# Kernel tuning notes

Measured on AMD Instinct MI355X. Metric: run time of the kernel, lower is better.

The kernel has to match this reference:

```python
import jax, jax.numpy as jnp
import numpy as np

N_QUBITS = 4
N_LAYERS = 2
ENT = [(i, (i + 1) % N_QUBITS) for i in range(N_QUBITS)]  # fixed entangling ring


def _ry(t):
    c, s = jnp.cos(t / 2), jnp.sin(t / 2)
    return jnp.stack([jnp.stack([c, -s]), jnp.stack([s, c])]).astype(jnp.complex64)


def _rx(t):
    c, s = jnp.cos(t / 2), jnp.sin(t / 2)
    return jnp.stack([jnp.stack([c + 0j, -1j * s]), jnp.stack([-1j * s, c + 0j])]).astype(jnp.complex64)


def _rz(t):
    e = jnp.exp(-0.5j * t.astype(jnp.complex64))
    z = jnp.zeros_like(e)
    return jnp.stack([jnp.stack([e, z]), jnp.stack([z, jnp.conj(e)])])


def _apply_1q(state, U, w):
    # state: (2,)*N_QUBITS; apply 2x2 U on wire w
    s = jnp.moveaxis(state, w, 0)
    s = jnp.tensordot(U, s, ((1,), (0,)))
    return jnp.moveaxis(s, 0, w)


def _cnot(state, c, t):
    s = jnp.moveaxis(state, (c, t), (0, 1))
    s = jnp.concatenate([s[:1], jnp.flip(s[1:], axis=1)], axis=0)
    return jnp.moveaxis(s, (0, 1), (c, t))


def _ansatz(state, vec, params):
    for i in range(N_QUBITS):
        state = _apply_1q(state, _ry(vec[i]), i)
    for l in range(N_LAYERS):
        for i in range(N_QUBITS):
            state = _apply_1q(state, _rx(params[l, i, 0]), i)
            state = _apply_1q(state, _ry(params[l, i, 1]), i)
            state = _apply_1q(state, _rz(params[l, i, 2]), i)
        for a_, b_ in ENT:
            state = _cnot(state, a_, b_)
    return state


def _adjoint_ansatz(state, vec, params):
    # inverse gates in reverse order
    for l in reversed(range(N_LAYERS)):
        for a_, b_ in reversed(ENT):
            state = _cnot(state, a_, b_)  # CNOT is self-inverse
        for i in reversed(range(N_QUBITS)):
            state = _apply_1q(state, _rz(-params[l, i, 2]), i)
            state = _apply_1q(state, _ry(-params[l, i, 1]), i)
            state = _apply_1q(state, _rx(-params[l, i, 0]), i)
    for i in reversed(range(N_QUBITS)):
        state = _apply_1q(state, _ry(-vec[i]), i)
    return state


def setup_inputs() -> dict:
    key = jax.random.key(0)
    k1, k2, k3 = jax.random.split(key, 3)
    a = jax.random.normal(k1, (1024, N_QUBITS), dtype=jnp.float32)
    b = jax.random.normal(k2, (1024, N_QUBITS), dtype=jnp.float32)
    params = jax.random.normal(k3, (N_LAYERS, N_QUBITS, 3), dtype=jnp.float32)
    return {"a": a, "b": b, "params": params}


def reference(a, b, params):
    def pair(x, y):
        psi = jnp.zeros((2,) * N_QUBITS, jnp.complex64).at[(0,) * N_QUBITS].set(1.0)
        psi = _ansatz(psi, x, params)
        psi = _adjoint_ansatz(psi, y, params)
        probs = jnp.abs(psi) ** 2
        # expval of PauliZ on wire 0: +1 for |0>, -1 for |1> on axis 0
        z = jnp.sum(probs[0]) - jnp.sum(probs[1])
        return jnp.abs(z)

    # Gram matrix [len(a), len(b)]
    return jax.vmap(lambda x: jax.vmap(lambda y: pair(x, y))(b))(a)
```

## Files before the change

### kernel.cpp

```cpp
#include <hip/hip_runtime.h>


#define NA 1024
#define NB 1024
#define KD 256
#define RT2 1.41421356237f

typedef __attribute__((ext_vector_type(8))) short bf16x8;
typedef __attribute__((ext_vector_type(4))) float f32x4;

__device__ __forceinline__ unsigned short f2bf(float x) {
    union { float f; unsigned u; } v; v.f = x;
    unsigned r = v.u + 0x7fffu + ((v.u >> 16) & 1u);
    return (unsigned short)(r >> 16);
}

__device__ __forceinline__ uint4 pack8(const float* f) {
    uint4 u;
    u.x = (unsigned)f2bf(f[0]) | ((unsigned)f2bf(f[1]) << 16);
    u.y = (unsigned)f2bf(f[2]) | ((unsigned)f2bf(f[3]) << 16);
    u.z = (unsigned)f2bf(f[4]) | ((unsigned)f2bf(f[5]) << 16);
    u.w = (unsigned)f2bf(f[6]) | ((unsigned)f2bf(f[7]) << 16);
    return u;
}

__device__ __forceinline__ void ry_gate(float* sr, float* si, int w, float t) {
    float s, c; __sincosf(0.5f * t, &s, &c);
    int st = 8 >> w;
    #pragma unroll
    for (int b = 0; b < 16; ++b) {
        if (b & st) continue;
        int j = b | st;
        float r0 = sr[b], i0 = si[b], r1 = sr[j], i1 = si[j];
        sr[b] = c * r0 - s * r1;  si[b] = c * i0 - s * i1;
        sr[j] = s * r0 + c * r1;  si[j] = s * i0 + c * i1;
    }
}

__device__ __forceinline__ void rx_gate(float* sr, float* si, int w, float t) {
    float s, c; __sincosf(0.5f * t, &s, &c);
    int st = 8 >> w;
    #pragma unroll
    for (int b = 0; b < 16; ++b) {
        if (b & st) continue;
        int j = b | st;
        float r0 = sr[b], i0 = si[b], r1 = sr[j], i1 = si[j];
        sr[b] = c * r0 + s * i1;  si[b] = c * i0 - s * r1;
        sr[j] = c * r1 + s * i0;  si[j] = c * i1 - s * r0;
    }
}

__device__ __forceinline__ void rz_gate(float* sr, float* si, int w, float t) {
    float s, c; __sincosf(0.5f * t, &s, &c);
    int st = 8 >> w;
    #pragma unroll
    for (int b = 0; b < 16; ++b) {
        if (b & st) continue;
        int j = b | st;
        float r0 = sr[b], i0 = si[b], r1 = sr[j], i1 = si[j];
        sr[b] = c * r0 + s * i0;  si[b] = c * i0 - s * r0;
        sr[j] = c * r1 - s * i1;  si[j] = c * i1 + s * r1;
    }
}

__device__ __forceinline__ void cnot_gate(float* sr, float* si, int cw, int tw) {
    int cs = 8 >> cw, ts = 8 >> tw;
    #pragma unroll
    for (int b = 0; b < 16; ++b) {
        if ((b & cs) && !(b & ts)) {
            int j = b | ts;
            float tr = sr[b]; sr[b] = sr[j]; sr[j] = tr;
            float ti = si[b]; si[b] = si[j]; si[j] = ti;
        }
    }
}

__device__ __forceinline__ void ansatz(float* sr, float* si, const float* vec, const float* P) {
    #pragma unroll
    for (int q = 0; q < 4; ++q) ry_gate(sr, si, q, vec[q]);
    #pragma unroll
    for (int l = 0; l < 2; ++l) {
        #pragma unroll
        for (int q = 0; q < 4; ++q) {
            rx_gate(sr, si, q, P[l * 12 + q * 3 + 0]);
            ry_gate(sr, si, q, P[l * 12 + q * 3 + 1]);
            rz_gate(sr, si, q, P[l * 12 + q * 3 + 2]);
        }
        cnot_gate(sr, si, 0, 1);
        cnot_gate(sr, si, 1, 2);
        cnot_gate(sr, si, 2, 3);
        cnot_gate(sr, si, 3, 0);
    }
}

__global__ __launch_bounds__(512, 2) void qkm_phase1(
    const float* __restrict__ a, const float* __restrict__ b,
    const float* __restrict__ params,
    uint4* __restrict__ Qv, uint4* __restrict__ Mv) {

    float P[24];
    #pragma unroll
    for (int j = 0; j < 24; ++j) P[j] = params[j];
    const int tid = threadIdx.x;
    const int blk = blockIdx.x;

    if (blk < 32) {
        __shared__ float Wtr[32 * 136];
        __shared__ float Wti[32 * 136];
        const int col0 = blk << 5;

        if (tid < 256) {
            const int y = tid >> 3, p2 = tid & 7;
            float sr[16], si[16];
            #pragma unroll
            for (int k = 0; k < 16; ++k) { sr[k] = (k == 8 + p2) ? 1.f : 0.f; si[k] = 0.f; }
            float vec[4];
            #pragma unroll
            for (int q = 0; q < 4; ++q) vec[q] = b[(col0 + y) * 4 + q];
            ansatz(sr, si, vec, P);
            float* wr = Wtr + y * 136 + p2 * 17;
            float* wi = Wti + y * 136 + p2 * 17;
            #pragma unroll
            for (int l = 0; l < 16; ++l) { wr[l] = sr[l]; wi[l] = si[l]; }
        }
        __syncthreads();

        const int y = tid >> 4, k = tid & 15;
        const float* wyr = Wtr + y * 136;
        const float* wyi = Wti + y * 136;
        float re[16], im[16];
        #pragma unroll
        for (int l = 0; l < 16; ++l) { re[l] = 0.f; im[l] = 0.f; }
        #pragma unroll
        for (int p2 = 0; p2 < 8; ++p2) {
            const float* br  = wyr + p2 * 17;
            const float* bi_ = wyi + p2 * 17;
            float ar = br[k], ai = bi_[k];
            #pragma unroll
            for (int l = 0; l < 16; ++l) {
                float xr = br[l], xi = bi_[l];
                re[l] += ar * xr + ai * xi;
                im[l] += xi * ar - xr * ai;
            }
        }
        float row[16];
        #pragma unroll
        for (int l = 0; l < 16; ++l) {
            float off = (l < k) ? im[l] : re[l];
            row[l] = (l == k) ? (1.f - 2.f * re[l]) : (-2.f * RT2 * off);
        }
        uint4* d = Mv + (size_t)(col0 + y) * 32 + k * 2;
        d[0] = pack8(row); d[1] = pack8(row + 8);
    } else {
        const int i = ((blk - 32) << 9) + tid;
        float sr[16], si[16];
        #pragma unroll
        for (int k = 0; k < 16; ++k) { sr[k] = (k == 0) ? 1.f : 0.f; si[k] = 0.f; }
        float vec[4];
        #pragma unroll
        for (int q = 0; q < 4; ++q) vec[q] = a[i * 4 + q];
        ansatz(sr, si, vec, P);
        #pragma unroll
        for (int k = 0; k < 16; ++k) {
            float rk = sr[k], ik = si[k];
            float row[16];
            #pragma unroll
            for (int l = 0; l < 16; ++l) {
                if (l < k)       row[l] = RT2 * (si[l] * rk - sr[l] * ik);
                else if (l == k) row[l] = rk * rk + ik * ik;
                else             row[l] = RT2 * (rk * sr[l] + ik * si[l]);
            }
            uint4* d = Qv + (size_t)i * 32 + k * 2;
            d[0] = pack8(row); d[1] = pack8(row + 8);
        }
    }
}

__global__ __launch_bounds__(256) void qkm_phase2(
    const unsigned short* __restrict__ Q, const unsigned short* __restrict__ M,
    float* __restrict__ out) {
    int wave = threadIdx.x >> 6;
    int lane = threadIdx.x & 63;
    int blk = blockIdx.x;
    int xcd = blk & 7;
    int slot = blk >> 3;
    int bi = xcd * 2 + (slot >> 4);
    int bj = slot & 15;
    int wi = wave >> 1, wj = wave & 1;
    int row0 = bi * 64 + wi * 32;
    int col0 = bj * 64 + wj * 32;
    int m16 = lane & 15;
    int quad = lane >> 4;

    const unsigned short* q0 = Q + (size_t)(row0 + m16) * KD + quad * 8;
    const unsigned short* q1 = q0 + 16 * KD;
    const unsigned short* m0 = M + (size_t)(col0 + m16) * KD + quad * 8;
    const unsigned short* m1 = m0 + 16 * KD;

    f32x4 a00 = {0.f,0.f,0.f,0.f}, a01 = {0.f,0.f,0.f,0.f};
    f32x4 a10 = {0.f,0.f,0.f,0.f}, a11 = {0.f,0.f,0.f,0.f};
    #pragma unroll
    for (int kk = 0; kk < 8; ++kk) {
        bf16x8 qa = *(const bf16x8*)(q0 + kk * 32);
        bf16x8 qb = *(const bf16x8*)(q1 + kk * 32);
        bf16x8 ma = *(const bf16x8*)(m0 + kk * 32);
        bf16x8 mb = *(const bf16x8*)(m1 + kk * 32);
        a00 = __builtin_amdgcn_mfma_f32_16x16x32_bf16(qa, ma, a00, 0, 0, 0);
        a01 = __builtin_amdgcn_mfma_f32_16x16x32_bf16(qa, mb, a01, 0, 0, 0);
        a10 = __builtin_amdgcn_mfma_f32_16x16x32_bf16(qb, ma, a10, 0, 0, 0);
        a11 = __builtin_amdgcn_mfma_f32_16x16x32_bf16(qb, mb, a11, 0, 0, 0);
    }
    #pragma unroll
    for (int r = 0; r < 4; ++r) {
        int r0o = row0 + quad * 4 + r;
        int r1o = r0o + 16;
        out[r0o * NB + col0 + m16]      = fabsf(a00[r]);
        out[r0o * NB + col0 + 16 + m16] = fabsf(a01[r]);
        out[r1o * NB + col0 + m16]      = fabsf(a10[r]);
        out[r1o * NB + col0 + 16 + m16] = fabsf(a11[r]);
    }
}

extern "C" void kernel_launch(void* const* d_in, const int* in_sizes, int n_in,
                              void* d_out, int out_size, void* d_ws, size_t ws_size,
                              hipStream_t stream) {
    const float* a = (const float*)d_in[0];
    const float* b = (const float*)d_in[1];
    const float* params = (const float*)d_in[2];
    float* out = (float*)d_out;

    unsigned short* Q = (unsigned short*)d_ws;
    unsigned short* M = Q + (size_t)NA * KD;

    qkm_phase1<<<34, 512, 0, stream>>>(a, b, params, (uint4*)Q, (uint4*)M);
    qkm_phase2<<<256, 256, 0, stream>>>(Q, M, out);
}
```

Before: 75.69 us.

## Spread phase-1 work over more small blocks and split phase-2 tiles across more waves

Phase 1 moves from 34 blocks of 512 threads to 72 blocks of 128 threads. Each B-block now handles 16 columns, and every thread in it computes two M rows. The goal is to spread the serial ansatz simulation over more CUs and so shorten the latency-bound first kernel. Phase 2 uses 8 waves per block instead of 4, each computing a 32x16 tile with 2 MFMAs instead of 32x32 with 4, which adds parallelism per block but reuses each loaded fragment less.

Measured after the change: 72.11 us. 1.05x faster.

```diff
diff --git a/kernel.cpp b/kernel.cpp
--- a/kernel.cpp
+++ b/kernel.cpp
@@ -93,7 +93,7 @@
     }
 }
 
-__global__ __launch_bounds__(512, 2) void qkm_phase1(
+__global__ __launch_bounds__(128, 1) void qkm_phase1(
     const float* __restrict__ a, const float* __restrict__ b,
     const float* __restrict__ params,
     uint4* __restrict__ Qv, uint4* __restrict__ Mv) {
@@ -104,61 +104,65 @@
     const int tid = threadIdx.x;
     const int blk = blockIdx.x;
 
-    if (blk < 32) {
-        __shared__ float Wtr[32 * 136];
-        __shared__ float Wti[32 * 136];
-        const int col0 = blk << 5;
-
-        if (tid < 256) {
-            const int y = tid >> 3, p2 = tid & 7;
+    if (blk < 64) {
+        __shared__ float Wtr[16 * 136];
+        __shared__ float Wti[16 * 136];
+        const int col0 = blk << 4;
+
+        {
+            const int yl = tid >> 3, p2 = tid & 7;
             float sr[16], si[16];
             #pragma unroll
             for (int k = 0; k < 16; ++k) { sr[k] = (k == 8 + p2) ? 1.f : 0.f; si[k] = 0.f; }
             float vec[4];
             #pragma unroll
-            for (int q = 0; q < 4; ++q) vec[q] = b[(col0 + y) * 4 + q];
+            for (int q = 0; q < 4; ++q) vec[q] = b[(size_t)(col0 + yl) * 4 + q];
             ansatz(sr, si, vec, P);
-            float* wr = Wtr + y * 136 + p2 * 17;
-            float* wi = Wti + y * 136 + p2 * 17;
+            float* wr = Wtr + yl * 136 + p2 * 17;
+            float* wi = Wti + yl * 136 + p2 * 17;
             #pragma unroll
             for (int l = 0; l < 16; ++l) { wr[l] = sr[l]; wi[l] = si[l]; }
         }
         __syncthreads();
 
-        const int y = tid >> 4, k = tid & 15;
-        const float* wyr = Wtr + y * 136;
-        const float* wyi = Wti + y * 136;
-        float re[16], im[16];
-        #pragma unroll
-        for (int l = 0; l < 16; ++l) { re[l] = 0.f; im[l] = 0.f; }
-        #pragma unroll
-        for (int p2 = 0; p2 < 8; ++p2) {
-            const float* br  = wyr + p2 * 17;
-            const float* bi_ = wyi + p2 * 17;
-            float ar = br[k], ai = bi_[k];
+        const int yl = tid >> 3, k0 = (tid & 7) << 1;
+        const float* wyr = Wtr + yl * 136;
+        const float* wyi = Wti + yl * 136;
+        #pragma unroll
+        for (int rr = 0; rr < 2; ++rr) {
+            const int k = k0 + rr;
+            float re[16], im[16];
+            #pragma unroll
+            for (int l = 0; l < 16; ++l) { re[l] = 0.f; im[l] = 0.f; }
+            #pragma unroll
+            for (int p2 = 0; p2 < 8; ++p2) {
+                const float* br  = wyr + p2 * 17;
+                const float* bi_ = wyi + p2 * 17;
+                float ar = br[k], ai = bi_[k];
+                #pragma unroll
+                for (int l = 0; l < 16; ++l) {
+                    float xr = br[l], xi = bi_[l];
+                    re[l] += ar * xr + ai * xi;
+                    im[l] += xi * ar - xr * ai;
+                }
+            }
+            float row[16];
             #pragma unroll
             for (int l = 0; l < 16; ++l) {
-                float xr = br[l], xi = bi_[l];
-                re[l] += ar * xr + ai * xi;
-                im[l] += xi * ar - xr * ai;
+                float off = (l < k) ? im[l] : re[l];
+                row[l] = (l == k) ? (1.f - 2.f * re[l]) : (-2.f * RT2 * off);
             }
-        }
-        float row[16];
-        #pragma unroll
-        for (int l = 0; l < 16; ++l) {
-            float off = (l < k) ? im[l] : re[l];
-            row[l] = (l == k) ? (1.f - 2.f * re[l]) : (-2.f * RT2 * off);
-        }
-        uint4* d = Mv + (size_t)(col0 + y) * 32 + k * 2;
-        d[0] = pack8(row); d[1] = pack8(row + 8);
+            uint4* d = Mv + (size_t)(col0 + yl) * 32 + k * 2;
+            d[0] = pack8(row); d[1] = pack8(row + 8);
+        }
     } else {
-        const int i = ((blk - 32) << 9) + tid;
+        const int i = ((blk - 64) << 7) + tid;
         float sr[16], si[16];
         #pragma unroll
         for (int k = 0; k < 16; ++k) { sr[k] = (k == 0) ? 1.f : 0.f; si[k] = 0.f; }
         float vec[4];
         #pragma unroll
-        for (int q = 0; q < 4; ++q) vec[q] = a[i * 4 + q];
+        for (int q = 0; q < 4; ++q) vec[q] = a[(size_t)i * 4 + q];
         ansatz(sr, si, vec, P);
         #pragma unroll
         for (int k = 0; k < 16; ++k) {
@@ -176,48 +180,37 @@
     }
 }
 
-__global__ __launch_bounds__(256) void qkm_phase2(
+__global__ __launch_bounds__(512, 2) void qkm_phase2(
     const unsigned short* __restrict__ Q, const unsigned short* __restrict__ M,
     float* __restrict__ out) {
-    int wave = threadIdx.x >> 6;
-    int lane = threadIdx.x & 63;
-    int blk = blockIdx.x;
-    int xcd = blk & 7;
-    int slot = blk >> 3;
-    int bi = xcd * 2 + (slot >> 4);
-    int bj = slot & 15;
-    int wi = wave >> 1, wj = wave & 1;
-    int row0 = bi * 64 + wi * 32;
-    int col0 = bj * 64 + wj * 32;
-    int m16 = lane & 15;
-    int quad = lane >> 4;
+    const int wave = threadIdx.x >> 6, lane = threadIdx.x & 63;
+    const int blk = blockIdx.x;
+    const int xcd = blk & 7, slot = blk >> 3;
+    const int bi = xcd * 2 + (slot >> 4);
+    const int bj = slot & 15;
+    const int wi = wave >> 2, wj = wave & 3;
+    const int row0 = bi * 64 + wi * 32;
+    const int col0 = bj * 64 + wj * 16;
+    const int m16 = lane & 15, quad = lane >> 4;
 
     const unsigned short* q0 = Q + (size_t)(row0 + m16) * KD + quad * 8;
     const unsigned short* q1 = q0 + 16 * KD;
     const unsigned short* m0 = M + (size_t)(col0 + m16) * KD + quad * 8;
-    const unsigned short* m1 = m0 + 16 * KD;
-
-    f32x4 a00 = {0.f,0.f,0.f,0.f}, a01 = {0.f,0.f,0.f,0.f};
-    f32x4 a10 = {0.f,0.f,0.f,0.f}, a11 = {0.f,0.f,0.f,0.f};
+
+    f32x4 a0 = {0.f, 0.f, 0.f, 0.f}, a1 = {0.f, 0.f, 0.f, 0.f};
     #pragma unroll
     for (int kk = 0; kk < 8; ++kk) {
         bf16x8 qa = *(const bf16x8*)(q0 + kk * 32);
         bf16x8 qb = *(const bf16x8*)(q1 + kk * 32);
         bf16x8 ma = *(const bf16x8*)(m0 + kk * 32);
-        bf16x8 mb = *(const bf16x8*)(m1 + kk * 32);
-        a00 = __builtin_amdgcn_mfma_f32_16x16x32_bf16(qa, ma, a00, 0, 0, 0);
-        a01 = __builtin_amdgcn_mfma_f32_16x16x32_bf16(qa, mb, a01, 0, 0, 0);
-        a10 = __builtin_amdgcn_mfma_f32_16x16x32_bf16(qb, ma, a10, 0, 0, 0);
-        a11 = __builtin_amdgcn_mfma_f32_16x16x32_bf16(qb, mb, a11, 0, 0, 0);
+        a0 = __builtin_amdgcn_mfma_f32_16x16x32_bf16(qa, ma, a0, 0, 0, 0);
+        a1 = __builtin_amdgcn_mfma_f32_16x16x32_bf16(qb, ma, a1, 0, 0, 0);
     }
     #pragma unroll
     for (int r = 0; r < 4; ++r) {
-        int r0o = row0 + quad * 4 + r;
-        int r1o = r0o + 16;
-        out[r0o * NB + col0 + m16]      = fabsf(a00[r]);
-        out[r0o * NB + col0 + 16 + m16] = fabsf(a01[r]);
-        out[r1o * NB + col0 + m16]      = fabsf(a10[r]);
-        out[r1o * NB + col0 + 16 + m16] = fabsf(a11[r]);
+        int orow = row0 + quad * 4 + r;
+        out[orow * NB + col0 + m16]        = fabsf(a0[r]);
+        out[(orow + 16) * NB + col0 + m16] = fabsf(a1[r]);
     }
 }
 
@@ -232,6 +225,6 @@
     unsigned short* Q = (unsigned short*)d_ws;
     unsigned short* M = Q + (size_t)NA * KD;
 
-    qkm_phase1<<<34, 512, 0, stream>>>(a, b, params, (uint4*)Q, (uint4*)M);
-    qkm_phase2<<<256, 256, 0, stream>>>(Q, M, out);
-}
+    qkm_phase1<<<72, 128, 0, stream>>>(a, b, params, (uint4*)Q, (uint4*)M);
+    qkm_phase2<<<256, 512, 0, stream>>>(Q, M, out);
+}
```
